# Optimization experiments

Measured on AMD Instinct MI355X. Metric: run time of the kernel, lower is better.

Reference implementation:

```python
import jax, jax.numpy as jnp
import numpy as np

BS, S, D, H = 4, 2048, 1024, 4096
TEMP, THRESH, PRIOR, EPS = 1.0, 0.5, 0.2, 1e-9


def setup_inputs() -> dict:
    key = jax.random.key(0)
    ks = jax.random.split(key, 4)
    hidden = jax.random.normal(ks[0], (BS, S, D), jnp.float32)
    # ragged valid lengths to exercise the padding / forced-last-boundary path
    lengths = jnp.array([S, S - 300, S - 700, S // 2], jnp.int32)
    attention_mask = (jnp.arange(S)[None, :] < lengths[:, None]).astype(jnp.float32)
    noise_u = jax.random.uniform(ks[1], (BS, S), jnp.float32, 1e-6, 1.0 - 1e-6)
    W1 = jax.random.normal(ks[2], (D, H), jnp.float32) * (1.0 / np.sqrt(D))
    b1 = jnp.zeros((H,), jnp.float32)
    W2 = jax.random.normal(ks[3], (H,), jnp.float32) * (1.0 / np.sqrt(H))
    b2 = jnp.zeros((), jnp.float32)
    return dict(hidden=hidden, attention_mask=attention_mask, noise_u=noise_u,
                W1=W1, b1=b1, W2=W2, b2=b2)


def reference(hidden, attention_mask, noise_u, W1, b1, W2, b2):
    bs, seq, _ = hidden.shape
    # tiny MLP gate -> per-token boundary logit
    h = jax.nn.relu(jnp.einsum('bsd,dh->bsh', hidden, W1) + b1)
    logits = jnp.einsum('bsh,h->bs', h, W2) + b2                     # [B,S]
    # RelaxedBernoulli(temp, probs=sigmoid(logits)).rsample()
    logistic = jnp.log(noise_u) - jnp.log1p(-noise_u)
    soft = jax.nn.sigmoid((logits + logistic) / TEMP)
    # straight-through hard boundaries
    hard = (soft > THRESH).astype(soft.dtype)
    hard = jax.lax.stop_gradient(hard - soft) + soft
    # mask out padding, force a boundary on the last real token of each row
    hard = hard * attention_mask
    pad = attention_mask == 0
    first_pad = pad & (jnp.cumsum(pad.astype(jnp.int32), axis=1) == 1)
    last_real = jnp.roll(first_pad, shift=-1, axis=1)
    last_real = last_real.at[:, -1].set(False)
    hard = jnp.maximum(hard, last_real.astype(hard.dtype))
    # downsample: mean-pool tokens within segments ending at boundary tokens
    hh1 = jnp.cumsum(hard, axis=1) - hard                            # [B,S] segment id of each token
    foo = jnp.arange(seq, dtype=hard.dtype)[None, None, :] - hh1[:, :, None]  # [B,S_tok,S_seg]
    lel = jnp.where(foo == 0, 1.0 - foo, 0.0)                        # one-hot (diff. via -foo)
    bar = lel / (jnp.sum(lel, axis=1, keepdims=True) + EPS)          # normalize per segment
    pooled = jnp.einsum('bld,bls->bsd', hidden, bar)                 # [B,S_seg,D] (zero-padded beyond max #segments)
    # binomial boundary-rate loss
    num_b = jnp.sum(hard)
    total = jnp.sum(attention_mask)
    gln = jax.scipy.special.gammaln
    log_prob = (gln(total + 1.0) - gln(num_b + 1.0) - gln(total - num_b + 1.0)
                + num_b * jnp.log(PRIOR) + (total - num_b) * jnp.log(1.0 - PRIOR))
    loss = -log_prob / total
    # shortened attention mask: kept positions all have mask==1, so it is a
    # left-packed ones mask of length = #boundaries per row (zero-padded to S)
    counts = jnp.sum(jax.lax.stop_gradient(hard), axis=1)
    short_mask = (jnp.arange(seq, dtype=counts.dtype)[None, :] < counts[:, None]).astype(jnp.float32)
    return pooled, loss, num_b, total, short_mask
```

## Files before the change

kernel.cpp:

```cpp
#include <hip/hip_runtime.h>
#include <math.h>

#define BSZ 4
#define SEQ 2048
#define DIM 1024
#define HID 4096
#define MTOT (BSZ * SEQ)
#define NHB 64
#define EPSF 1e-9f

#define BM 256
#define BN 256
#define BKF 32
#define KITERS (DIM / BKF)
#define BSCALE 32.0f
#define INV_BSCALE (1.0f / 32.0f)

typedef _Float16 f16;
typedef _Float16 f16x4 __attribute__((ext_vector_type(4)));
typedef _Float16 f16x8 __attribute__((ext_vector_type(8)));
typedef float f32x16 __attribute__((ext_vector_type(16)));

__device__ __forceinline__ void gl16(const f16* g, f16* l) {
  __builtin_amdgcn_global_load_lds(
      (const __attribute__((address_space(1))) void*)g,
      (__attribute__((address_space(3))) void*)l, 16, 0, 0);
}

__global__ void split_a(const float* __restrict__ in, f16* __restrict__ hi,
                        f16* __restrict__ lo) {
  int i = blockIdx.x * 256 + threadIdx.x;
  float4 v = ((const float4*)in)[i];
  f16x4 h, l;
  h.x = (f16)v.x; h.y = (f16)v.y; h.z = (f16)v.z; h.w = (f16)v.w;
  l.x = (f16)(v.x - (float)h.x);
  l.y = (f16)(v.y - (float)h.y);
  l.z = (f16)(v.z - (float)h.z);
  l.w = (f16)(v.w - (float)h.w);
  ((f16x4*)hi)[i] = h;
  ((f16x4*)lo)[i] = l;
}

__global__ void split_w1t(const float* __restrict__ w1, f16* __restrict__ hi,
                          f16* __restrict__ lo) {
  __shared__ float tile[32][36];
  const int k0 = blockIdx.x * 32;
  const int h0 = blockIdx.y * 32;
  const int t = threadIdx.x;
  {
    int kk = t >> 3, hq = (t & 7) * 4;
    float4 v = *(const float4*)&w1[(size_t)(k0 + kk) * HID + h0 + hq];
    tile[kk][hq + 0] = v.x; tile[kk][hq + 1] = v.y;
    tile[kk][hq + 2] = v.z; tile[kk][hq + 3] = v.w;
  }
  __syncthreads();
  int hh = t >> 3, kq = (t & 7) * 4;
  f16x4 H, L;
#pragma unroll
  for (int j = 0; j < 4; ++j) {
    float x = tile[kq + j][hh] * BSCALE;
    f16 xh = (f16)x;
    H[j] = xh;
    L[j] = (f16)(x - (float)xh);
  }
  *(f16x4*)&hi[(size_t)(h0 + hh) * DIM + k0 + kq] = H;
  *(f16x4*)&lo[(size_t)(h0 + hh) * DIM + k0 + kq] = L;
}

__global__ __launch_bounds__(512, 2)
void gate_gemm(const f16* __restrict__ Ahi, const f16* __restrict__ Alo,
               const f16* __restrict__ Whi, const f16* __restrict__ Wlo,
               const float* __restrict__ b1, const float* __restrict__ W2,
               float* __restrict__ partial) {
  __shared__ f16 sA[2][BM][64];
  __shared__ f16 sB[2][BN][64];

  const int bid = blockIdx.x;
  const int wg = (bid & 7) * 64 + (bid >> 3);
  const int nt = wg >> 5;
  const int mt = wg & 31;
  const int m0 = mt * BM, h0 = nt * BN;

  const int t = threadIdx.x;
  const int lane = t & 63, wid = t >> 6;
  const int wm = wid >> 2, wn = wid & 3;
  const int rowl = lane & 31, kb = lane >> 5;

  f32x16 acc[4][2];
#pragma unroll
  for (int a = 0; a < 4; ++a)
#pragma unroll
    for (int b = 0; b < 2; ++b)
#pragma unroll
      for (int e = 0; e < 16; ++e) acc[a][b][e] = 0.f;

  const f16* srcA[4];
  const f16* srcB[4];
#pragma unroll
  for (int i = 0; i < 4; ++i) {
    int sig = i * 512 + t;
    int r = sig >> 3, p = sig & 7;
    int q = p ^ (r & 7);
    int koff = (q & 3) * 8;
    srcA[i] = (q < 4 ? Ahi : Alo) + (size_t)(m0 + r) * DIM + koff;
    srcB[i] = (q < 4 ? Whi : Wlo) + (size_t)(h0 + r) * DIM + koff;
  }

#define STAGE(buf, kt)                                                        \
  {                                                                           \
    _Pragma("unroll") for (int i = 0; i < 4; ++i) {                           \
      int ho = (i * 512 + wid * 64) * 8;                                      \
      gl16(srcA[i] + (size_t)(kt) * BKF, &sA[buf][0][0] + ho);                \
      gl16(srcB[i] + (size_t)(kt) * BKF, &sB[buf][0][0] + ho);                \
    }                                                                         \
  }

  STAGE(0, 0);
  __syncthreads();

  for (int kt = 0; kt < KITERS; ++kt) {
    const int buf = kt & 1;
    if (kt + 1 < KITERS) STAGE(buf ^ 1, kt + 1);
#pragma unroll
    for (int ks = 0; ks < 2; ++ks) {
      f16x8 ah[4], al[4], bh[2], bl[2];
      const int sl = ks * 2 + kb;
#pragma unroll
      for (int fm = 0; fm < 4; ++fm) {
        int ra = wm * 128 + fm * 32 + rowl;
        int ph = (sl ^ (ra & 7)) * 8;
        ah[fm] = *(const f16x8*)&sA[buf][ra][ph];
        al[fm] = *(const f16x8*)&sA[buf][ra][ph ^ 32];
      }
#pragma unroll
      for (int fn = 0; fn < 2; ++fn) {
        int rb = wn * 64 + fn * 32 + rowl;
        int pb = (sl ^ (rb & 7)) * 8;
        bh[fn] = *(const f16x8*)&sB[buf][rb][pb];
        bl[fn] = *(const f16x8*)&sB[buf][rb][pb ^ 32];
      }
#pragma unroll
      for (int fm = 0; fm < 4; ++fm)
#pragma unroll
        for (int fn = 0; fn < 2; ++fn)
          acc[fm][fn] = __builtin_amdgcn_mfma_f32_32x32x16_f16(
              ah[fm], bh[fn], acc[fm][fn], 0, 0, 0);
#pragma unroll
      for (int fm = 0; fm < 4; ++fm)
#pragma unroll
        for (int fn = 0; fn < 2; ++fn)
          acc[fm][fn] = __builtin_amdgcn_mfma_f32_32x32x16_f16(
              ah[fm], bl[fn], acc[fm][fn], 0, 0, 0);
#pragma unroll
      for (int fm = 0; fm < 4; ++fm)
#pragma unroll
        for (int fn = 0; fn < 2; ++fn)
          acc[fm][fn] = __builtin_amdgcn_mfma_f32_32x32x16_f16(
              al[fm], bh[fn], acc[fm][fn], 0, 0, 0);
    }
    __syncthreads();
  }

  float b1v[2], w2v[2];
#pragma unroll
  for (int fn = 0; fn < 2; ++fn) {
    int h = h0 + wn * 64 + fn * 32 + rowl;
    b1v[fn] = b1[h];
    w2v[fn] = W2[h];
  }
#pragma unroll
  for (int fm = 0; fm < 4; ++fm)
#pragma unroll
    for (int r = 0; r < 16; ++r) {
      float v0 = acc[fm][0][r] * INV_BSCALE + b1v[0];
      float v1 = acc[fm][1][r] * INV_BSCALE + b1v[1];
      acc[fm][0][r] = fmaxf(v0, 0.f) * w2v[0] + fmaxf(v1, 0.f) * w2v[1];
    }
#pragma unroll
  for (int off = 1; off <= 16; off <<= 1)
#pragma unroll
    for (int fm = 0; fm < 4; ++fm)
#pragma unroll
      for (int r = 0; r < 16; ++r)
        acc[fm][0][r] += __shfl_xor(acc[fm][0][r], off);
  if (rowl == 0) {
    const int hb = nt * 4 + wn;
#pragma unroll
    for (int fm = 0; fm < 4; ++fm)
#pragma unroll
      for (int r = 0; r < 16; ++r) {
        int token = m0 + wm * 128 + fm * 32 + (r & 3) + 8 * (r >> 2) + 4 * kb;
        partial[(size_t)hb * MTOT + token] = acc[fm][0][r];
      }
  }
}

__global__ void reduce_logits(const float* __restrict__ partial,
                              float* __restrict__ logits) {
  int s = blockIdx.x * 256 + threadIdx.x;
  float lg = 0.f;
#pragma unroll
  for (int h = 0; h < NHB; ++h) lg += partial[(size_t)h * MTOT + s];
  logits[s] = lg;
}

__global__ void boundary_scan(const float* __restrict__ logits,
                              const float* __restrict__ mask,
                              const float* __restrict__ noise,
                              const float* __restrict__ b2,
                              int* __restrict__ bpos, int* __restrict__ counts,
                              int* __restrict__ lengths,
                              float* __restrict__ shortmask) {
  const int b = blockIdx.x;
  const int t = threadIdx.x;
  __shared__ float hardS[SEQ];
  __shared__ float red[256];
  const float bias2 = b2[0];

  float msum = 0.f;
  for (int s = t; s < SEQ; s += 256) {
    float lg = logits[b * SEQ + s] + bias2;
    float u = noise[b * SEQ + s];
    float lgt = logf(u) - log1pf(-u);
    float m = mask[b * SEQ + s];
    float hard = ((lg + lgt) > 0.f) ? 1.f : 0.f;
    hardS[s] = hard * m;
    msum += m;
  }
  red[t] = msum;
  __syncthreads();
  for (int off = 128; off > 0; off >>= 1) {
    if (t < off) red[t] += red[t + off];
    __syncthreads();
  }
  int L = (int)(red[0] + 0.5f);
  __syncthreads();
  if (t == 0) {
    if (L < SEQ) hardS[L - 1] = fmaxf(hardS[L - 1], 1.f);
    lengths[b] = L;
  }
  __syncthreads();

  float loc[8];
  float run = 0.f;
#pragma unroll
  for (int i = 0; i < 8; ++i) { loc[i] = hardS[t * 8 + i]; run += loc[i]; }
  red[t] = run;
  __syncthreads();
  for (int off = 1; off < 256; off <<= 1) {
    float v = (t >= off) ? red[t - off] : 0.f;
    __syncthreads();
    red[t] += v;
    __syncthreads();
  }
  float base = red[t] - run;
  int cnt = (int)(red[255] + 0.5f);

  float pre = base;
#pragma unroll
  for (int i = 0; i < 8; ++i) {
    if (loc[i] > 0.5f) {
      int rank = (int)(pre + 0.5f);
      bpos[b * SEQ + rank] = t * 8 + i;
    }
    pre += loc[i];
  }
  if (t == 0) counts[b] = cnt;
  for (int s = t; s < SEQ; s += 256)
    shortmask[b * SEQ + s] = (s < cnt) ? 1.f : 0.f;
}

__global__ void pool_seg(const float* __restrict__ hidden,
                         const int* __restrict__ bpos,
                         const int* __restrict__ counts,
                         float* __restrict__ pooled) {
  const int g = blockIdx.x, b = blockIdx.y;
  const int t = threadIdx.x;
  const int cnt = counts[b];
  float4 acc = {0.f, 0.f, 0.f, 0.f};
  float* outp = pooled + ((size_t)(b * SEQ + g)) * DIM + t * 4;
  if (g > cnt) { *(float4*)outp = acc; return; }
  if (g == cnt) return;
  int start = (g == 0) ? 0 : bpos[b * SEQ + g - 1] + 1;
  int end = bpos[b * SEQ + g] + 1;
  const float* hb = hidden + ((size_t)b * SEQ) * DIM + t * 4;
  for (int l = start; l < end; ++l) {
    float4 v = *(const float4*)(hb + (size_t)l * DIM);
    acc.x += v.x; acc.y += v.y; acc.z += v.z; acc.w += v.w;
  }
  float inv = 1.f / ((float)(end - start) + EPSF);
  acc.x *= inv; acc.y *= inv; acc.z *= inv; acc.w *= inv;
  *(float4*)outp = acc;
}

__global__ void pool_tail_partial(const float* __restrict__ hidden,
                                  const int* __restrict__ bpos,
                                  const int* __restrict__ counts,
                                  float* __restrict__ tailpart) {
  const int c = blockIdx.x;
  const int b = blockIdx.y;
  const int t = threadIdx.x;
  int cnt = counts[b];
  int start = (cnt == 0) ? 0 : bpos[b * SEQ + cnt - 1] + 1;
  int n = SEQ - start;
  int clen = (n + 15) / 16;
  int s0 = start + c * clen;
  int s1 = s0 + clen; if (s1 > SEQ) s1 = SEQ;
  float4 acc = {0.f, 0.f, 0.f, 0.f};
  const float* hb = hidden + ((size_t)b * SEQ) * DIM + t * 4;
  for (int l = s0; l < s1; ++l) {
    float4 v = *(const float4*)(hb + (size_t)l * DIM);
    acc.x += v.x; acc.y += v.y; acc.z += v.z; acc.w += v.w;
  }
  *(float4*)(tailpart + ((size_t)(b * 16 + c)) * DIM + t * 4) = acc;
}

__global__ void pool_tail_final(const int* __restrict__ bpos,
                                const int* __restrict__ counts,
                                const float* __restrict__ tailpart,
                                float* __restrict__ pooled) {
  const int b = blockIdx.x;
  const int t = threadIdx.x;
  int cnt = counts[b];
  if (cnt >= SEQ) return;
  int start = (cnt == 0) ? 0 : bpos[b * SEQ + cnt - 1] + 1;
  float4 acc = {0.f, 0.f, 0.f, 0.f};
  for (int c = 0; c < 16; ++c) {
    float4 v = *(const float4*)(tailpart + ((size_t)(b * 16 + c)) * DIM + t * 4);
    acc.x += v.x; acc.y += v.y; acc.z += v.z; acc.w += v.w;
  }
  float inv = 1.f / ((float)(SEQ - start) + EPSF);
  acc.x *= inv; acc.y *= inv; acc.z *= inv; acc.w *= inv;
  *(float4*)(pooled + ((size_t)(b * SEQ + cnt)) * DIM + t * 4) = acc;
}

__global__ void loss_kernel(const int* __restrict__ counts,
                            const int* __restrict__ lengths,
                            float* __restrict__ outScalars) {
  if (threadIdx.x != 0 || blockIdx.x != 0) return;
  double num_b = 0.0, total = 0.0;
  for (int b = 0; b < BSZ; ++b) { num_b += (double)counts[b]; total += (double)lengths[b]; }
  double lp = lgamma(total + 1.0) - lgamma(num_b + 1.0) - lgamma(total - num_b + 1.0)
            + num_b * log(0.2) + (total - num_b) * log(0.8);
  outScalars[0] = (float)(-lp / total);
  outScalars[1] = (float)num_b;
  outScalars[2] = (float)total;
}

extern "C" void kernel_launch(void* const* d_in, const int* in_sizes, int n_in,
                              void* d_out, int out_size, void* d_ws, size_t ws_size,
                              hipStream_t stream) {
  const float* hidden = (const float*)d_in[0];
  const float* mask   = (const float*)d_in[1];
  const float* noise  = (const float*)d_in[2];
  const float* W1     = (const float*)d_in[3];
  const float* b1     = (const float*)d_in[4];
  const float* W2     = (const float*)d_in[5];
  const float* b2     = (const float*)d_in[6];

  float* out = (float*)d_out;
  float* pooled = out;
  float* scalars = out + (size_t)BSZ * SEQ * DIM;
  float* shortmask = scalars + 3;

  char* ws = (char*)d_ws;
  size_t off = 0;
  float* partial = (float*)(ws + off); off += (size_t)NHB * MTOT * sizeof(float);
  f16* Ahi = (f16*)(ws + off); off += (size_t)MTOT * DIM * sizeof(f16);
  f16* Alo = (f16*)(ws + off); off += (size_t)MTOT * DIM * sizeof(f16);
  f16* Whi = (f16*)(ws + off); off += (size_t)HID * DIM * sizeof(f16);
  f16* Wlo = (f16*)(ws + off); off += (size_t)HID * DIM * sizeof(f16);
  float* logits = (float*)(ws + off); off += (size_t)MTOT * sizeof(float);
  int* bpos = (int*)(ws + off); off += (size_t)BSZ * SEQ * sizeof(int);
  int* counts = (int*)(ws + off); off += 16 * sizeof(int);
  int* lengths = (int*)(ws + off); off += 16 * sizeof(int);
  off = (off + 255) & ~(size_t)255;
  float* tailpart = (float*)(ws + off);

  split_a<<<MTOT * DIM / 4 / 256, 256, 0, stream>>>(hidden, Ahi, Alo);
  split_w1t<<<dim3(DIM / 32, HID / 32), 256, 0, stream>>>(W1, Whi, Wlo);
  gate_gemm<<<(MTOT / BM) * (HID / BN), 512, 0, stream>>>(Ahi, Alo, Whi, Wlo,
                                                          b1, W2, partial);
  reduce_logits<<<MTOT / 256, 256, 0, stream>>>(partial, logits);
  boundary_scan<<<BSZ, 256, 0, stream>>>(logits, mask, noise, b2,
                                         bpos, counts, lengths, shortmask);
  pool_tail_partial<<<dim3(16, BSZ), 256, 0, stream>>>(hidden, bpos, counts, tailpart);
  pool_seg<<<dim3(SEQ, BSZ), 256, 0, stream>>>(hidden, bpos, counts, pooled);
  pool_tail_final<<<BSZ, 256, 0, stream>>>(bpos, counts, tailpart, pooled);
  loss_kernel<<<1, 1, 0, stream>>>(counts, lengths, scalars);
}
```

Measured before the change: 271.6 us.

## Shrink GEMM tiles to 128x128 and fuse auxiliary kernels to cut launches

The gate GEMM tile shrinks from 256x256 with 512 threads to 128x128 with 256 threads, giving four times as many workgroups and a remapped block swizzle. The two f16 split kernels merge into one launch with 8-wide vectors. The logit reduction moves into boundary_scan, the loss computation into pool_tail_partial, and the tail finalisation into pool_seg, removing four small launches. Smaller tiles lower data reuse per workgroup and raise LDS and global traffic in the GEMM. NHB stays at 64, which still matches 32 column tiles times 2 warps, but boundary_scan now sums 64 partials on only 4 blocks.

```diff
diff --git a/kernel.cpp b/kernel.cpp
--- a/kernel.cpp
+++ b/kernel.cpp
@@ -9,8 +9,8 @@
 #define NHB 64
 #define EPSF 1e-9f
 
-#define BM 256
-#define BN 256
+#define BM 128
+#define BN 128
 #define BKF 32
 #define KITERS (DIM / BKF)
 #define BSCALE 32.0f
@@ -27,26 +27,33 @@
       (__attribute__((address_space(3))) void*)l, 16, 0, 0);
 }
 
-__global__ void split_a(const float* __restrict__ in, f16* __restrict__ hi,
-                        f16* __restrict__ lo) {
-  int i = blockIdx.x * 256 + threadIdx.x;
-  float4 v = ((const float4*)in)[i];
-  f16x4 h, l;
-  h.x = (f16)v.x; h.y = (f16)v.y; h.z = (f16)v.z; h.w = (f16)v.w;
-  l.x = (f16)(v.x - (float)h.x);
-  l.y = (f16)(v.y - (float)h.y);
-  l.z = (f16)(v.z - (float)h.z);
-  l.w = (f16)(v.w - (float)h.w);
-  ((f16x4*)hi)[i] = h;
-  ((f16x4*)lo)[i] = l;
-}
-
-__global__ void split_w1t(const float* __restrict__ w1, f16* __restrict__ hi,
-                          f16* __restrict__ lo) {
+#define NA_BLOCKS (MTOT * DIM / 8 / 256)
+#define NW_BLOCKS ((DIM / 32) * (HID / 32))
+
+__global__ void split_all(const float* __restrict__ inA, f16* __restrict__ Ahi,
+                          f16* __restrict__ Alo, const float* __restrict__ w1,
+                          f16* __restrict__ Whi, f16* __restrict__ Wlo) {
   __shared__ float tile[32][36];
-  const int k0 = blockIdx.x * 32;
-  const int h0 = blockIdx.y * 32;
-  const int t = threadIdx.x;
+  const int bid = blockIdx.x;
+  const int t = threadIdx.x;
+  if (bid < NA_BLOCKS) {
+    int i = bid * 256 + t;
+    const float4* inp = (const float4*)inA + (size_t)i * 2;
+    float4 v0 = inp[0], v1 = inp[1];
+    f16x8 h, l;
+    h[0] = (f16)v0.x; h[1] = (f16)v0.y; h[2] = (f16)v0.z; h[3] = (f16)v0.w;
+    h[4] = (f16)v1.x; h[5] = (f16)v1.y; h[6] = (f16)v1.z; h[7] = (f16)v1.w;
+    l[0] = (f16)(v0.x - (float)h[0]); l[1] = (f16)(v0.y - (float)h[1]);
+    l[2] = (f16)(v0.z - (float)h[2]); l[3] = (f16)(v0.w - (float)h[3]);
+    l[4] = (f16)(v1.x - (float)h[4]); l[5] = (f16)(v1.y - (float)h[5]);
+    l[6] = (f16)(v1.z - (float)h[6]); l[7] = (f16)(v1.w - (float)h[7]);
+    ((f16x8*)Ahi)[i] = h;
+    ((f16x8*)Alo)[i] = l;
+    return;
+  }
+  const int wb = bid - NA_BLOCKS;
+  const int k0 = (wb & 31) * 32;
+  const int h0 = (wb >> 5) * 32;
   {
     int kk = t >> 3, hq = (t & 7) * 4;
     float4 v = *(const float4*)&w1[(size_t)(k0 + kk) * HID + h0 + hq];
@@ -63,11 +70,11 @@
     H[j] = xh;
     L[j] = (f16)(x - (float)xh);
   }
-  *(f16x4*)&hi[(size_t)(h0 + hh) * DIM + k0 + kq] = H;
-  *(f16x4*)&lo[(size_t)(h0 + hh) * DIM + k0 + kq] = L;
-}
-
-__global__ __launch_bounds__(512, 2)
+  *(f16x4*)&Whi[(size_t)(h0 + hh) * DIM + k0 + kq] = H;
+  *(f16x4*)&Wlo[(size_t)(h0 + hh) * DIM + k0 + kq] = L;
+}
+
+__global__ __launch_bounds__(256, 2)
 void gate_gemm(const f16* __restrict__ Ahi, const f16* __restrict__ Alo,
                const f16* __restrict__ Whi, const f16* __restrict__ Wlo,
                const float* __restrict__ b1, const float* __restrict__ W2,
@@ -76,19 +83,19 @@
   __shared__ f16 sB[2][BN][64];
 
   const int bid = blockIdx.x;
-  const int wg = (bid & 7) * 64 + (bid >> 3);
-  const int nt = wg >> 5;
-  const int mt = wg & 31;
+  const int wg = (bid & 7) * 256 + (bid >> 3);
+  const int nt = wg >> 6;
+  const int mt = wg & 63;
   const int m0 = mt * BM, h0 = nt * BN;
 
   const int t = threadIdx.x;
   const int lane = t & 63, wid = t >> 6;
-  const int wm = wid >> 2, wn = wid & 3;
+  const int wm = wid >> 1, wn = wid & 1;
   const int rowl = lane & 31, kb = lane >> 5;
 
-  f32x16 acc[4][2];
-#pragma unroll
-  for (int a = 0; a < 4; ++a)
+  f32x16 acc[2][2];
+#pragma unroll
+  for (int a = 0; a < 2; ++a)
 #pragma unroll
     for (int b = 0; b < 2; ++b)
 #pragma unroll
@@ -98,7 +105,7 @@
   const f16* srcB[4];
 #pragma unroll
   for (int i = 0; i < 4; ++i) {
-    int sig = i * 512 + t;
+    int sig = i * 256 + t;
     int r = sig >> 3, p = sig & 7;
     int q = p ^ (r & 7);
     int koff = (q & 3) * 8;
@@ -106,14 +113,12 @@
     srcB[i] = (q < 4 ? Whi : Wlo) + (size_t)(h0 + r) * DIM + koff;
   }
 
-#define STAGE(buf, kt)                                                        \
-  {                                                                           \
-    _Pragma("unroll") for (int i = 0; i < 4; ++i) {                           \
-      int ho = (i * 512 + wid * 64) * 8;                                      \
-      gl16(srcA[i] + (size_t)(kt) * BKF, &sA[buf][0][0] + ho);                \
-      gl16(srcB[i] + (size_t)(kt) * BKF, &sB[buf][0][0] + ho);                \
-    }                                                                         \
-  }
+#define STAGE(buf_, kt_)                                                      \
+  { _Pragma("unroll") for (int i = 0; i < 4; ++i) {                           \
+      int ho = (i * 256 + wid * 64) * 8;                                      \
+      gl16(srcA[i] + (size_t)(kt_) * BKF, &sA[buf_][0][0] + ho);              \
+      gl16(srcB[i] + (size_t)(kt_) * BKF, &sB[buf_][0][0] + ho);              \
+  } }
 
   STAGE(0, 0);
   __syncthreads();
@@ -123,11 +128,11 @@
     if (kt + 1 < KITERS) STAGE(buf ^ 1, kt + 1);
 #pragma unroll
     for (int ks = 0; ks < 2; ++ks) {
-      f16x8 ah[4], al[4], bh[2], bl[2];
+      f16x8 ah[2], al[2], bh[2], bl[2];
       const int sl = ks * 2 + kb;
 #pragma unroll
-      for (int fm = 0; fm < 4; ++fm) {
-        int ra = wm * 128 + fm * 32 + rowl;
+      for (int fm = 0; fm < 2; ++fm) {
+        int ra = wm * 64 + fm * 32 + rowl;
         int ph = (sl ^ (ra & 7)) * 8;
         ah[fm] = *(const f16x8*)&sA[buf][ra][ph];
         al[fm] = *(const f16x8*)&sA[buf][ra][ph ^ 32];
@@ -140,19 +145,19 @@
         bl[fn] = *(const f16x8*)&sB[buf][rb][pb ^ 32];
       }
 #pragma unroll
-      for (int fm = 0; fm < 4; ++fm)
+      for (int fm = 0; fm < 2; ++fm)
 #pragma unroll
         for (int fn = 0; fn < 2; ++fn)
           acc[fm][fn] = __builtin_amdgcn_mfma_f32_32x32x16_f16(
               ah[fm], bh[fn], acc[fm][fn], 0, 0, 0);
 #pragma unroll
-      for (int fm = 0; fm < 4; ++fm)
+      for (int fm = 0; fm < 2; ++fm)
 #pragma unroll
         for (int fn = 0; fn < 2; ++fn)
           acc[fm][fn] = __builtin_amdgcn_mfma_f32_32x32x16_f16(
               ah[fm], bl[fn], acc[fm][fn], 0, 0, 0);
 #pragma unroll
-      for (int fm = 0; fm < 4; ++fm)
+      for (int fm = 0; fm < 2; ++fm)
 #pragma unroll
         for (int fn = 0; fn < 2; ++fn)
           acc[fm][fn] = __builtin_amdgcn_mfma_f32_32x32x16_f16(
@@ -169,7 +174,7 @@
     w2v[fn] = W2[h];
   }
 #pragma unroll
-  for (int fm = 0; fm < 4; ++fm)
+  for (int fm = 0; fm < 2; ++fm)
 #pragma unroll
     for (int r = 0; r < 16; ++r) {
       float v0 = acc[fm][0][r] * INV_BSCALE + b1v[0];
@@ -179,32 +184,23 @@
 #pragma unroll
   for (int off = 1; off <= 16; off <<= 1)
 #pragma unroll
-    for (int fm = 0; fm < 4; ++fm)
+    for (int fm = 0; fm < 2; ++fm)
 #pragma unroll
       for (int r = 0; r < 16; ++r)
         acc[fm][0][r] += __shfl_xor(acc[fm][0][r], off);
   if (rowl == 0) {
-    const int hb = nt * 4 + wn;
-#pragma unroll
-    for (int fm = 0; fm < 4; ++fm)
+    const int hb = nt * 2 + wn;
+#pragma unroll
+    for (int fm = 0; fm < 2; ++fm)
 #pragma unroll
       for (int r = 0; r < 16; ++r) {
-        int token = m0 + wm * 128 + fm * 32 + (r & 3) + 8 * (r >> 2) + 4 * kb;
+        int token = m0 + wm * 64 + fm * 32 + (r & 3) + 8 * (r >> 2) + 4 * kb;
         partial[(size_t)hb * MTOT + token] = acc[fm][0][r];
       }
   }
 }
 
-__global__ void reduce_logits(const float* __restrict__ partial,
-                              float* __restrict__ logits) {
-  int s = blockIdx.x * 256 + threadIdx.x;
-  float lg = 0.f;
-#pragma unroll
-  for (int h = 0; h < NHB; ++h) lg += partial[(size_t)h * MTOT + s];
-  logits[s] = lg;
-}
-
-__global__ void boundary_scan(const float* __restrict__ logits,
+__global__ void boundary_scan(const float* __restrict__ partial,
                               const float* __restrict__ mask,
                               const float* __restrict__ noise,
                               const float* __restrict__ b2,
@@ -219,7 +215,9 @@
 
   float msum = 0.f;
   for (int s = t; s < SEQ; s += 256) {
-    float lg = logits[b * SEQ + s] + bias2;
+    float lg = bias2;
+#pragma unroll
+    for (int h = 0; h < NHB; ++h) lg += partial[(size_t)h * MTOT + b * SEQ + s];
     float u = noise[b * SEQ + s];
     float lgt = logf(u) - log1pf(-u);
     float m = mask[b * SEQ + s];
@@ -270,33 +268,12 @@
     shortmask[b * SEQ + s] = (s < cnt) ? 1.f : 0.f;
 }
 
-__global__ void pool_seg(const float* __restrict__ hidden,
-                         const int* __restrict__ bpos,
-                         const int* __restrict__ counts,
-                         float* __restrict__ pooled) {
-  const int g = blockIdx.x, b = blockIdx.y;
-  const int t = threadIdx.x;
-  const int cnt = counts[b];
-  float4 acc = {0.f, 0.f, 0.f, 0.f};
-  float* outp = pooled + ((size_t)(b * SEQ + g)) * DIM + t * 4;
-  if (g > cnt) { *(float4*)outp = acc; return; }
-  if (g == cnt) return;
-  int start = (g == 0) ? 0 : bpos[b * SEQ + g - 1] + 1;
-  int end = bpos[b * SEQ + g] + 1;
-  const float* hb = hidden + ((size_t)b * SEQ) * DIM + t * 4;
-  for (int l = start; l < end; ++l) {
-    float4 v = *(const float4*)(hb + (size_t)l * DIM);
-    acc.x += v.x; acc.y += v.y; acc.z += v.z; acc.w += v.w;
-  }
-  float inv = 1.f / ((float)(end - start) + EPSF);
-  acc.x *= inv; acc.y *= inv; acc.z *= inv; acc.w *= inv;
-  *(float4*)outp = acc;
-}
-
 __global__ void pool_tail_partial(const float* __restrict__ hidden,
                                   const int* __restrict__ bpos,
                                   const int* __restrict__ counts,
-                                  float* __restrict__ tailpart) {
+                                  const int* __restrict__ lengths,
+                                  float* __restrict__ tailpart,
+                                  float* __restrict__ outScalars) {
   const int c = blockIdx.x;
   const int b = blockIdx.y;
   const int t = threadIdx.x;
@@ -313,38 +290,54 @@
     acc.x += v.x; acc.y += v.y; acc.z += v.z; acc.w += v.w;
   }
   *(float4*)(tailpart + ((size_t)(b * 16 + c)) * DIM + t * 4) = acc;
-}
-
-__global__ void pool_tail_final(const int* __restrict__ bpos,
-                                const int* __restrict__ counts,
-                                const float* __restrict__ tailpart,
-                                float* __restrict__ pooled) {
-  const int b = blockIdx.x;
-  const int t = threadIdx.x;
-  int cnt = counts[b];
-  if (cnt >= SEQ) return;
-  int start = (cnt == 0) ? 0 : bpos[b * SEQ + cnt - 1] + 1;
+
+  if (c == 0 && b == 0 && t == 0) {
+    double num_b = 0.0, total = 0.0;
+    for (int bb = 0; bb < BSZ; ++bb) {
+      num_b += (double)counts[bb];
+      total += (double)lengths[bb];
+    }
+    double lp = lgamma(total + 1.0) - lgamma(num_b + 1.0)
+              - lgamma(total - num_b + 1.0)
+              + num_b * log(0.2) + (total - num_b) * log(0.8);
+    outScalars[0] = (float)(-lp / total);
+    outScalars[1] = (float)num_b;
+    outScalars[2] = (float)total;
+  }
+}
+
+__global__ void pool_seg(const float* __restrict__ hidden,
+                         const int* __restrict__ bpos,
+                         const int* __restrict__ counts,
+                         const float* __restrict__ tailpart,
+                         float* __restrict__ pooled) {
+  const int g = blockIdx.x, b = blockIdx.y;
+  const int t = threadIdx.x;
+  const int cnt = counts[b];
   float4 acc = {0.f, 0.f, 0.f, 0.f};
-  for (int c = 0; c < 16; ++c) {
-    float4 v = *(const float4*)(tailpart + ((size_t)(b * 16 + c)) * DIM + t * 4);
+  float* outp = pooled + ((size_t)(b * SEQ + g)) * DIM + t * 4;
+  if (g > cnt) { *(float4*)outp = acc; return; }
+  if (g == cnt) {
+    int start = (cnt == 0) ? 0 : bpos[b * SEQ + cnt - 1] + 1;
+    for (int c = 0; c < 16; ++c) {
+      float4 v = *(const float4*)(tailpart + ((size_t)(b * 16 + c)) * DIM + t * 4);
+      acc.x += v.x; acc.y += v.y; acc.z += v.z; acc.w += v.w;
+    }
+    float inv = 1.f / ((float)(SEQ - start) + EPSF);
+    acc.x *= inv; acc.y *= inv; acc.z *= inv; acc.w *= inv;
+    *(float4*)outp = acc;
+    return;
+  }
+  int start = (g == 0) ? 0 : bpos[b * SEQ + g - 1] + 1;
+  int end = bpos[b * SEQ + g] + 1;
+  const float* hb = hidden + ((size_t)b * SEQ) * DIM + t * 4;
+  for (int l = start; l < end; ++l) {
+    float4 v = *(const float4*)(hb + (size_t)l * DIM);
     acc.x += v.x; acc.y += v.y; acc.z += v.z; acc.w += v.w;
   }
-  float inv = 1.f / ((float)(SEQ - start) + EPSF);
+  float inv = 1.f / ((float)(end - start) + EPSF);
   acc.x *= inv; acc.y *= inv; acc.z *= inv; acc.w *= inv;
-  *(float4*)(pooled + ((size_t)(b * SEQ + cnt)) * DIM + t * 4) = acc;
-}
-
-__global__ void loss_kernel(const int* __restrict__ counts,
-                            const int* __restrict__ lengths,
-                            float* __restrict__ outScalars) {
-  if (threadIdx.x != 0 || blockIdx.x != 0) return;
-  double num_b = 0.0, total = 0.0;
-  for (int b = 0; b < BSZ; ++b) { num_b += (double)counts[b]; total += (double)lengths[b]; }
-  double lp = lgamma(total + 1.0) - lgamma(num_b + 1.0) - lgamma(total - num_b + 1.0)
-            + num_b * log(0.2) + (total - num_b) * log(0.8);
-  outScalars[0] = (float)(-lp / total);
-  outScalars[1] = (float)num_b;
-  outScalars[2] = (float)total;
+  *(float4*)outp = acc;
 }
 
 extern "C" void kernel_launch(void* const* d_in, const int* in_sizes, int n_in,
@@ -370,22 +363,20 @@
   f16* Alo = (f16*)(ws + off); off += (size_t)MTOT * DIM * sizeof(f16);
   f16* Whi = (f16*)(ws + off); off += (size_t)HID * DIM * sizeof(f16);
   f16* Wlo = (f16*)(ws + off); off += (size_t)HID * DIM * sizeof(f16);
-  float* logits = (float*)(ws + off); off += (size_t)MTOT * sizeof(float);
   int* bpos = (int*)(ws + off); off += (size_t)BSZ * SEQ * sizeof(int);
   int* counts = (int*)(ws + off); off += 16 * sizeof(int);
   int* lengths = (int*)(ws + off); off += 16 * sizeof(int);
   off = (off + 255) & ~(size_t)255;
   float* tailpart = (float*)(ws + off);
 
-  split_a<<<MTOT * DIM / 4 / 256, 256, 0, stream>>>(hidden, Ahi, Alo);
-  split_w1t<<<dim3(DIM / 32, HID / 32), 256, 0, stream>>>(W1, Whi, Wlo);
-  gate_gemm<<<(MTOT / BM) * (HID / BN), 512, 0, stream>>>(Ahi, Alo, Whi, Wlo,
+  split_all<<<NA_BLOCKS + NW_BLOCKS, 256, 0, stream>>>(hidden, Ahi, Alo,
+                                                       W1, Whi, Wlo);
+  gate_gemm<<<(MTOT / BM) * (HID / BN), 256, 0, stream>>>(Ahi, Alo, Whi, Wlo,
                                                           b1, W2, partial);
-  reduce_logits<<<MTOT / 256, 256, 0, stream>>>(partial, logits);
-  boundary_scan<<<BSZ, 256, 0, stream>>>(logits, mask, noise, b2,
+  boundary_scan<<<BSZ, 256, 0, stream>>>(partial, mask, noise, b2,
                                          bpos, counts, lengths, shortmask);
-  pool_tail_partial<<<dim3(16, BSZ), 256, 0, stream>>>(hidden, bpos, counts, tailpart);
-  pool_seg<<<dim3(SEQ, BSZ), 256, 0, stream>>>(hidden, bpos, counts, pooled);
-  pool_tail_final<<<BSZ, 256, 0, stream>>>(bpos, counts, tailpart, pooled);
-  loss_kernel<<<1, 1, 0, stream>>>(counts, lengths, scalars);
-}
+  pool_tail_partial<<<dim3(16, BSZ), 256, 0, stream>>>(hidden, bpos, counts,
+                                                       lengths, tailpart, scalars);
+  pool_seg<<<dim3(SEQ, BSZ), 256, 0, stream>>>(hidden, bpos, counts,
+                                               tailpart, pooled);
+}
```

Measured after the change: 287.7 us. 1.06x slower.
